# Kernel optimization log

Hardware: AMD Instinct MI355X
Metric: run time of the kernel (lower is better)

## Reference

```python
import jax, jax.numpy as jnp
import numpy as np

TEMPERATURE = 0.1
NUM_POS = 2


def _cross_entropy(logits, labels):
    # mean over batch of -log_softmax(logits)[i, labels[i]]
    logp = jax.nn.log_softmax(logits, axis=-1)
    return -jnp.take_along_axis(logp, labels[:, None], axis=1).mean()


def setup_inputs() -> dict:
    key = jax.random.key(0)
    k1, k2, k3 = jax.random.split(key, 3)
    B, D, Q = 4096, 256, 65536
    embedding = jax.random.normal(k1, (B, D), dtype=jnp.float32)
    preds = jax.random.normal(k2, (B, D), dtype=jnp.float32)
    queue = jax.random.normal(k3, (Q, D), dtype=jnp.float32)
    queue = queue / jnp.linalg.norm(queue, axis=1, keepdims=True)
    return {"embedding": embedding, "preds": preds, "queue": queue}


def reference(embedding, preds, queue):
    B = embedding.shape[0]
    half = B // NUM_POS
    labels = jnp.arange(half)  # single-trainer: dist_rank = 0

    # nearest-neighbor retrieval from the support queue (no-grad in original)
    sim = embedding @ queue.T                      # [B, Q]
    nearest = queue[jnp.argmax(sim, axis=1)]       # [B, D]

    nn_a, nn_b = nearest[:half], nearest[half:]
    preds_a, preds_b = preds[:half], preds[half:]

    logits_ab = (nn_a @ preds_b.T) / TEMPERATURE   # [half, half]
    logits_ba = (nn_b @ preds_a.T) / TEMPERATURE

    loss = _cross_entropy(logits_ab, labels) / 2 + _cross_entropy(logits_ba, labels) / 2
    return loss
```

## Files before the change

kernel.cpp:

```cpp
#include <hip/hip_runtime.h>
#include <hip/hip_bf16.h>
#include <stdint.h>

#define B_ROWS 4096
#define D_K    256
#define Q_ROWS 65536
#define HALF   2048

typedef __bf16 bf16x8 __attribute__((ext_vector_type(8)));
typedef float  f32x4  __attribute__((ext_vector_type(4)));
typedef int    v8i    __attribute__((ext_vector_type(8)));
typedef int    v4i    __attribute__((ext_vector_type(4)));
typedef unsigned short u16x8 __attribute__((ext_vector_type(8)));
typedef const __attribute__((address_space(1))) void* gptr1;
typedef __attribute__((address_space(3))) void* lptr3;

__device__ __forceinline__ unsigned int f32_ordered(float f) {
    unsigned int u = __float_as_uint(f);
    return (u & 0x80000000u) ? ~u : (u | 0x80000000u);
}

__device__ __forceinline__ unsigned short f2bf_rn(float f) {
    unsigned int u = __float_as_uint(f);
    u += 0x7FFFu + ((u >> 16) & 1u);
    return (unsigned short)(u >> 16);
}

#define EMB4  (B_ROWS * D_K / 4)
#define PRED4 (B_ROWS * D_K / 4)
#define QUE4  (Q_ROWS * D_K / 4)
#define PREP_THREADS ((EMB4 + PRED4 + QUE4) / 4)
__global__ __launch_bounds__(256) void prep_kernel(const float* __restrict__ emb,
                                                   const float* __restrict__ preds,
                                                   const float* __restrict__ queue,
                                                   unsigned char* __restrict__ emb8,
                                                   unsigned short* __restrict__ preds_bf,
                                                   unsigned char* __restrict__ queue8,
                                                   unsigned long long* __restrict__ amax,
                                                   float* __restrict__ out) {
    const int t  = blockIdx.x * 256 + threadIdx.x;
    const int g0 = t * 4;
    if (g0 < EMB4) {
        const float4* src = (const float4*)emb + g0;
        int4 o;
        { float4 v = src[0]; int u = __builtin_amdgcn_cvt_pk_fp8_f32(v.x, v.y, 0, false);
          o.x = __builtin_amdgcn_cvt_pk_fp8_f32(v.z, v.w, u, true); }
        { float4 v = src[1]; int u = __builtin_amdgcn_cvt_pk_fp8_f32(v.x, v.y, 0, false);
          o.y = __builtin_amdgcn_cvt_pk_fp8_f32(v.z, v.w, u, true); }
        { float4 v = src[2]; int u = __builtin_amdgcn_cvt_pk_fp8_f32(v.x, v.y, 0, false);
          o.z = __builtin_amdgcn_cvt_pk_fp8_f32(v.z, v.w, u, true); }
        { float4 v = src[3]; int u = __builtin_amdgcn_cvt_pk_fp8_f32(v.x, v.y, 0, false);
          o.w = __builtin_amdgcn_cvt_pk_fp8_f32(v.z, v.w, u, true); }
        ((int4*)emb8)[t] = o;
    } else if (g0 < EMB4 + PRED4) {
        const int off = g0 - EMB4;
        const float4* src = (const float4*)preds + off;
#pragma unroll
        for (int h = 0; h < 2; h++) {
            float4 v0 = src[2 * h], v1 = src[2 * h + 1];
            u16x8 o;
            o[0] = f2bf_rn(v0.x); o[1] = f2bf_rn(v0.y); o[2] = f2bf_rn(v0.z); o[3] = f2bf_rn(v0.w);
            o[4] = f2bf_rn(v1.x); o[5] = f2bf_rn(v1.y); o[6] = f2bf_rn(v1.z); o[7] = f2bf_rn(v1.w);
            ((u16x8*)preds_bf)[(off >> 1) + h] = o;
        }
    } else {
        const int off = g0 - EMB4 - PRED4;
        const float4* src = (const float4*)queue + off;
        int4 o;
        { float4 v = src[0]; int u = __builtin_amdgcn_cvt_pk_fp8_f32(v.x, v.y, 0, false);
          o.x = __builtin_amdgcn_cvt_pk_fp8_f32(v.z, v.w, u, true); }
        { float4 v = src[1]; int u = __builtin_amdgcn_cvt_pk_fp8_f32(v.x, v.y, 0, false);
          o.y = __builtin_amdgcn_cvt_pk_fp8_f32(v.z, v.w, u, true); }
        { float4 v = src[2]; int u = __builtin_amdgcn_cvt_pk_fp8_f32(v.x, v.y, 0, false);
          o.z = __builtin_amdgcn_cvt_pk_fp8_f32(v.z, v.w, u, true); }
        { float4 v = src[3]; int u = __builtin_amdgcn_cvt_pk_fp8_f32(v.x, v.y, 0, false);
          o.w = __builtin_amdgcn_cvt_pk_fp8_f32(v.z, v.w, u, true); }
        ((int4*)queue8)[off >> 2] = o;
    }
    if (t < B_ROWS) amax[t] = 0ull;
    if (t == 0) out[0] = 0.f;
}

#define BM 128
#define BN 128
#define NCHUNK 8
#define MFMA_FP8(av, bv, c) \
    __builtin_amdgcn_mfma_scale_f32_16x16x128_f8f6f4((av), (bv), (c), 0, 0, 0, 0x7F7F7F7F, 0, 0x7F7F7F7F)

#define WAITV(N) asm volatile("s_waitcnt vmcnt(" #N ")" ::: "memory")
#define BARRIER() do { __builtin_amdgcn_s_barrier(); \
                       asm volatile("" ::: "memory"); \
                       __builtin_amdgcn_sched_barrier(0); } while (0)

__global__ __launch_bounds__(256, 2) void sim_argmax_kernel(const unsigned char* __restrict__ A8,
                                                            const unsigned char* __restrict__ B8,
                                                            unsigned long long* __restrict__ amax) {
    __shared__ unsigned char sh[49152];

    const int tid  = threadIdx.x;
    const int wave = tid >> 6;
    const int lane = tid & 63;
    const int l15  = lane & 15;
    const int quad = lane >> 4;

    const int bid  = blockIdx.x;
    const int xcd  = bid & 7;
    const int j    = bid >> 3;
    const int blk_m = (j & 31) * BM;
    const int ngrp  = (j >> 5) * 8 + xcd;
    const int nbase = ngrp * (BN * NCHUNK);

    const int wave_m = (wave >> 1) * 64;
    const int wave_n = (wave & 1) * 64;

    {
        const unsigned char* gA = A8 + (size_t)(blk_m + (tid >> 4)) * D_K
                                     + (((tid & 15) ^ ((tid >> 4) & 15)) << 4);
#pragma unroll
        for (int jj = 0; jj < 8; jj++)
            __builtin_amdgcn_global_load_lds((gptr1)(gA + jj * 4096),
                                             (lptr3)&sh[jj * 4096 + wave * 1024], 16, 0, 0);
    }
    __syncthreads();

    const int pA = (quad * 2) ^ l15;
    v8i areg[2][4];
#pragma unroll
    for (int kt = 0; kt < 2; kt++) {
#pragma unroll
        for (int mi = 0; mi < 4; mi++) {
            const int _lo = (wave_m + mi * 16 + l15) * 256 + ((pA ^ (kt << 3)) << 4);
            v4i _x = *(const v4i*)&sh[_lo];
            v4i _y = *(const v4i*)&sh[_lo ^ 16];
            areg[kt][mi] = __builtin_shufflevector(_x, _y, 0, 1, 2, 3, 4, 5, 6, 7);
        }
    }
    __syncthreads();

    if ((bid >> 8) & 1) {
        __builtin_amdgcn_s_sleep(8);
        __builtin_amdgcn_s_sleep(4);
    }

    const unsigned char* gB = B8 + (size_t)(nbase + (tid >> 3)) * D_K
                                 + (((tid & 7) ^ ((tid >> 3) & 7)) << 4);

#define PREFB(T, BSOFF) do {                                                           \
        const int _off = ((T) >> 1) * (32 * D_K * 4) + ((T) & 1) * 128;                \
        _Pragma("unroll")                                                              \
        for (int _j = 0; _j < 4; _j++)                                                 \
            __builtin_amdgcn_global_load_lds((gptr1)(gB + _j * 8192 + _off),           \
                                             (lptr3)&sh[(BSOFF) + _j * 4096 + wave * 1024], 16, 0, 0); \
    } while (0)

    int Bbase[4];
#pragma unroll
    for (int ni = 0; ni < 4; ni++) Bbase[ni] = (wave_n + ni * 16 + l15) * 128;
    const int pB = (quad * 2) ^ (l15 & 7);

    int bestk[4][4];
#pragma unroll
    for (int mi = 0; mi < 4; mi++)
#pragma unroll
        for (int reg = 0; reg < 4; reg++) bestk[mi][reg] = 0x80000000;

    f32x4 acc[4][4];
    const f32x4 zero4 = (f32x4){0.f, 0.f, 0.f, 0.f};

#define COMPUTE0(BSOFF) do {                                                           \
        __builtin_amdgcn_s_setprio(1);                                                 \
        _Pragma("unroll")                                                              \
        for (int ni = 0; ni < 4; ni++) {                                               \
            const int _lo = (BSOFF) + Bbase[ni] + (pB << 4);                           \
            v4i _x = *(const v4i*)&sh[_lo];                                            \
            v4i _y = *(const v4i*)&sh[_lo ^ 16];                                       \
            v8i bv = __builtin_shufflevector(_x, _y, 0, 1, 2, 3, 4, 5, 6, 7);          \
            _Pragma("unroll")                                                          \
            for (int mi = 0; mi < 4; mi++)                                             \
                acc[mi][ni] = MFMA_FP8(areg[0][mi], bv, zero4);                        \
        }                                                                              \
        __builtin_amdgcn_s_setprio(0);                                                 \
    } while (0)

#define COMPUTE1(BSOFF) do {                                                           \
        __builtin_amdgcn_s_setprio(1);                                                 \
        _Pragma("unroll")                                                              \
        for (int ni = 0; ni < 4; ni++) {                                               \
            const int _lo = (BSOFF) + Bbase[ni] + (pB << 4);                           \
            v4i _x = *(const v4i*)&sh[_lo];                                            \
            v4i _y = *(const v4i*)&sh[_lo ^ 16];                                       \
            v8i bv = __builtin_shufflevector(_x, _y, 0, 1, 2, 3, 4, 5, 6, 7);          \
            _Pragma("unroll")                                                          \
            for (int mi = 0; mi < 4; mi++)                                             \
                acc[mi][ni] = MFMA_FP8(areg[1][mi], bv, acc[mi][ni]);                  \
        }                                                                              \
        __builtin_amdgcn_s_setprio(0);                                                 \
    } while (0)

#define FOLDK(PP) do {                                                                 \
        _Pragma("unroll")                                                              \
        for (int ni = 0; ni < 4; ni++) {                                               \
            const int _slot = 31 - ((PP) * 4 + ni);      \
            _Pragma("unroll")                                                          \
            for (int mi = 0; mi < 4; mi++)                                             \
                _Pragma("unroll")                                                      \
                for (int reg = 0; reg < 4; reg++) {                                    \
                    int ik = (__float_as_int(acc[mi][ni][reg]) & 0xFFFFFFE0) | _slot;  \
                    bestk[mi][reg] = max(bestk[mi][reg], ik);                          \
                }                                                                      \
        }                                                                              \
    } while (0)

#define ROT() do { int _t = b0; b0 = b1; b1 = b2; b2 = _t; } while (0)

    int b0 = 0, b1 = 16384, b2 = 32768;

    PREFB(0, b0);
    PREFB(1, b1);

#pragma unroll 1
    for (int p = 0; p < NCHUNK; ++p) {
        WAITV(4); BARRIER();
        if (p < NCHUNK - 1) PREFB(2 * p + 2, b2);
        if (p > 0) FOLDK(p - 1);
        COMPUTE0(b0);
        ROT();
        if (p < NCHUNK - 1) { WAITV(4); } else { WAITV(0); }
        BARRIER();
        if (p < NCHUNK - 1) PREFB(2 * p + 3, b2);
        COMPUTE1(b0);
        ROT();
    }
    FOLDK(NCHUNK - 1);

#pragma unroll
    for (int mi = 0; mi < 4; mi++) {
#pragma unroll
        for (int reg = 0; reg < 4; reg++) {
            unsigned u     = (unsigned)bestk[mi][reg];
            unsigned vbits = u & 0xFFFFFFE0u;
            int      pni   = 31 - (int)(u & 31u);
            int      col   = nbase + (pni >> 2) * BN + wave_n + ((pni & 3) << 4) + l15;
            unsigned ov    = (vbits & 0x80000000u) ? ~vbits : (vbits | 0x80000000u);
            unsigned long long key =
                ((unsigned long long)ov << 32) |
                (unsigned long long)(0xFFFFFFFFu - (unsigned)col);
#pragma unroll
            for (int m = 1; m < 16; m <<= 1) {
                unsigned long long o = __shfl_xor(key, m, 16);
                if (o > key) key = o;
            }
            if (l15 == mi * 4 + reg) {
                int row = blk_m + wave_m + mi * 16 + quad * 4 + reg;
                atomicMax(&amax[row], key);
            }
        }
    }
}

__global__ __launch_bounds__(512) void logits_ce_kernel(const unsigned long long* __restrict__ amax,
                                                        const float* __restrict__ queue_f32,
                                                        const unsigned short* __restrict__ preds_bf,
                                                        float* __restrict__ out) {
    const int gw   = blockIdx.x;
    const int tid  = threadIdx.x;
    const int wave = tid >> 6;
    const int lane = tid & 63;
    const int l15  = lane & 15;
    const int quad = lane >> 4;
    const int h    = gw >> 7;
    const int rowbase = gw * 16;
    const unsigned short* Bbase = preds_bf + (size_t)((1 - h) * HALF) * D_K;

    __shared__ float sm[8][16], sl[8][16], sd[8][16];

    unsigned idx = 0xFFFFFFFFu - (unsigned)(amax[rowbase + l15] & 0xFFFFFFFFull);
    const float* arow = queue_f32 + (size_t)idx * D_K;
    bf16x8 a[8];
#pragma unroll
    for (int kc = 0; kc < 8; kc++) {
        float4 f0 = *(const float4*)(arow + kc * 32 + quad * 8);
        float4 f1 = *(const float4*)(arow + kc * 32 + quad * 8 + 4);
        u16x8 t;
        t[0] = f2bf_rn(f0.x); t[1] = f2bf_rn(f0.y); t[2] = f2bf_rn(f0.z); t[3] = f2bf_rn(f0.w);
        t[4] = f2bf_rn(f1.x); t[5] = f2bf_rn(f1.y); t[6] = f2bf_rn(f1.z); t[7] = f2bf_rn(f1.w);
        a[kc] = *(const bf16x8*)&t;
    }

    float m_run[4], l_run[4], diag[4];
#pragma unroll
    for (int r = 0; r < 4; r++) { m_run[r] = -1e30f; l_run[r] = 0.f; diag[r] = -1e30f; }

    const int tdiag = gw & 127;
    for (int tt = 0; tt < 16; tt++) {
        const int t = wave * 16 + tt;
        f32x4 acc0 = (f32x4){0.f, 0.f, 0.f, 0.f};
        f32x4 acc1 = (f32x4){0.f, 0.f, 0.f, 0.f};
#pragma unroll
        for (int kc = 0; kc < 4; kc++) {
            bf16x8 b0 = *(const bf16x8*)&Bbase[(size_t)(t * 16 + l15) * D_K + kc * 32 + quad * 8];
            acc0 = __builtin_amdgcn_mfma_f32_16x16x32_bf16(a[kc], b0, acc0, 0, 0, 0);
            bf16x8 b1 = *(const bf16x8*)&Bbase[(size_t)(t * 16 + l15) * D_K + (kc + 4) * 32 + quad * 8];
            acc1 = __builtin_amdgcn_mfma_f32_16x16x32_bf16(a[kc + 4], b1, acc1, 0, 0, 0);
        }
        f32x4 acc = acc0 + acc1;
#pragma unroll
        for (int reg = 0; reg < 4; reg++) {
            float v = acc[reg] * 10.0f;
            if (t == tdiag && l15 == quad * 4 + reg) diag[reg] = v;
            float nm = fmaxf(m_run[reg], v);
            l_run[reg] = l_run[reg] * __expf(m_run[reg] - nm) + __expf(v - nm);
            m_run[reg] = nm;
        }
    }
#pragma unroll
    for (int reg = 0; reg < 4; reg++) {
#pragma unroll
        for (int m = 1; m < 16; m <<= 1) {
            float om = __shfl_xor(m_run[reg], m, 16);
            float ol = __shfl_xor(l_run[reg], m, 16);
            float od = __shfl_xor(diag[reg], m, 16);
            float nm = fmaxf(m_run[reg], om);
            l_run[reg] = l_run[reg] * __expf(m_run[reg] - nm) + ol * __expf(om - nm);
            m_run[reg] = nm;
            diag[reg] = fmaxf(diag[reg], od);
        }
        if (l15 == 0) {
            sm[wave][quad * 4 + reg] = m_run[reg];
            sl[wave][quad * 4 + reg] = l_run[reg];
            sd[wave][quad * 4 + reg] = diag[reg];
        }
    }
    __syncthreads();
    if (tid < 16) {
        float M = -1e30f, L = 0.f, Dg = -1e30f;
#pragma unroll
        for (int w = 0; w < 8; w++) {
            float mw = sm[w][tid], lw = sl[w][tid], dw = sd[w][tid];
            float nM = fmaxf(M, mw);
            L = L * __expf(M - nM) + lw * __expf(mw - nM);
            M = nM;
            Dg = fmaxf(Dg, dw);
        }
        float rl = (M + __logf(L)) - Dg;
#pragma unroll
        for (int m = 1; m < 16; m <<= 1) rl += __shfl_xor(rl, m, 16);
        if (tid == 0) atomicAdd(out, rl * (1.0f / (float)B_ROWS));
    }
}

extern "C" void kernel_launch(void* const* d_in, const int* in_sizes, int n_in,
                              void* d_out, int out_size, void* d_ws, size_t ws_size,
                              hipStream_t stream) {
    const float* emb   = (const float*)d_in[0];
    const float* preds = (const float*)d_in[1];
    const float* queue = (const float*)d_in[2];

    char* w = (char*)d_ws;
    unsigned long long* amax  = (unsigned long long*)w;
    unsigned char*  emb8      = (unsigned char*)(w + (1u << 20));
    unsigned short* preds_bf  = (unsigned short*)(w + (2u << 20));
    unsigned char*  queue8    = (unsigned char*)(w + (4u << 20));

    prep_kernel<<<dim3(PREP_THREADS / 256), 256, 0, stream>>>(
        emb, preds, queue, emb8, preds_bf, queue8, amax, (float*)d_out);
    sim_argmax_kernel<<<dim3((B_ROWS / BM) * (Q_ROWS / (BN * NCHUNK))), 256, 0, stream>>>(
        emb8, queue8, amax);
    logits_ce_kernel<<<dim3(B_ROWS / 16), 512, 0, stream>>>(
        amax, queue, preds_bf, (float*)d_out);
}
```

Before: 210.0 us.

## Load B fragments directly from global into registers, dropping LDS staging

Replaces the triple-buffered global_load_lds staging of queue tiles, along with its barriers and waitcnts, with direct per-lane global loads into register double buffers b0/b1 that feed the FP8 MFMAs. LDS shrinks to only what the A tile needs, and the staggered sleep for odd block groups is removed. This aims to cut LDS traffic and barrier synchronisation, and the smaller LDS footprint may allow more blocks per CU. In exchange, B data is no longer shared across the two wave rows, so each wave fetches its own copy from global/L2. The 32-byte per-lane loads are less coalesced, so load latency may be exposed behind less lookahead.

```diff
diff --git a/kernel.cpp b/kernel.cpp
--- a/kernel.cpp
+++ b/kernel.cpp
@@ -87,15 +87,10 @@
 #define MFMA_FP8(av, bv, c) \
     __builtin_amdgcn_mfma_scale_f32_16x16x128_f8f6f4((av), (bv), (c), 0, 0, 0, 0x7F7F7F7F, 0, 0x7F7F7F7F)
 
-#define WAITV(N) asm volatile("s_waitcnt vmcnt(" #N ")" ::: "memory")
-#define BARRIER() do { __builtin_amdgcn_s_barrier(); \
-                       asm volatile("" ::: "memory"); \
-                       __builtin_amdgcn_sched_barrier(0); } while (0)
-
 __global__ __launch_bounds__(256, 2) void sim_argmax_kernel(const unsigned char* __restrict__ A8,
                                                             const unsigned char* __restrict__ B8,
                                                             unsigned long long* __restrict__ amax) {
-    __shared__ unsigned char sh[49152];
+    __shared__ unsigned char sh[32768];
 
     const int tid  = threadIdx.x;
     const int wave = tid >> 6;
@@ -135,28 +130,11 @@
             areg[kt][mi] = __builtin_shufflevector(_x, _y, 0, 1, 2, 3, 4, 5, 6, 7);
         }
     }
-    __syncthreads();
-
-    if ((bid >> 8) & 1) {
-        __builtin_amdgcn_s_sleep(8);
-        __builtin_amdgcn_s_sleep(4);
-    }
-
-    const unsigned char* gB = B8 + (size_t)(nbase + (tid >> 3)) * D_K
-                                 + (((tid & 7) ^ ((tid >> 3) & 7)) << 4);
-
-#define PREFB(T, BSOFF) do {                                                           \
-        const int _off = ((T) >> 1) * (32 * D_K * 4) + ((T) & 1) * 128;                \
-        _Pragma("unroll")                                                              \
-        for (int _j = 0; _j < 4; _j++)                                                 \
-            __builtin_amdgcn_global_load_lds((gptr1)(gB + _j * 8192 + _off),           \
-                                             (lptr3)&sh[(BSOFF) + _j * 4096 + wave * 1024], 16, 0, 0); \
-    } while (0)
-
-    int Bbase[4];
-#pragma unroll
-    for (int ni = 0; ni < 4; ni++) Bbase[ni] = (wave_n + ni * 16 + l15) * 128;
-    const int pB = (quad * 2) ^ (l15 & 7);
+
+    const unsigned char* bptr0 = B8 + (size_t)(nbase + wave_n + l15) * 256 + quad * 32;
+    const unsigned char* bptr[4];
+#pragma unroll
+    for (int ni = 0; ni < 4; ni++) bptr[ni] = bptr0 + ni * 16 * 256;
 
     int bestk[4][4];
 #pragma unroll
@@ -167,14 +145,27 @@
     f32x4 acc[4][4];
     const f32x4 zero4 = (f32x4){0.f, 0.f, 0.f, 0.f};
 
-#define COMPUTE0(BSOFF) do {                                                           \
+    v4i b0[8], b1[8];
+
+#define LOADH(BUF, KT) do {                                                            \
+        _Pragma("unroll")                                                              \
+        for (int ni = 0; ni < 4; ni++) {                                               \
+            BUF[2 * ni]     = *(const v4i*)(bptr[ni] + (KT) * 128);                    \
+            BUF[2 * ni + 1] = *(const v4i*)(bptr[ni] + (KT) * 128 + 16);               \
+        }                                                                              \
+    } while (0)
+
+#define ADVB() do {                                                                    \
+        _Pragma("unroll")                                                              \
+        for (int ni = 0; ni < 4; ni++) bptr[ni] += BN * D_K;           \
+    } while (0)
+
+#define COMPUTE0(BUF) do {                                                             \
         __builtin_amdgcn_s_setprio(1);                                                 \
         _Pragma("unroll")                                                              \
         for (int ni = 0; ni < 4; ni++) {                                               \
-            const int _lo = (BSOFF) + Bbase[ni] + (pB << 4);                           \
-            v4i _x = *(const v4i*)&sh[_lo];                                            \
-            v4i _y = *(const v4i*)&sh[_lo ^ 16];                                       \
-            v8i bv = __builtin_shufflevector(_x, _y, 0, 1, 2, 3, 4, 5, 6, 7);          \
+            v8i bv = __builtin_shufflevector(BUF[2 * ni], BUF[2 * ni + 1],             \
+                                             0, 1, 2, 3, 4, 5, 6, 7);                  \
             _Pragma("unroll")                                                          \
             for (int mi = 0; mi < 4; mi++)                                             \
                 acc[mi][ni] = MFMA_FP8(areg[0][mi], bv, zero4);                        \
@@ -182,14 +173,12 @@
         __builtin_amdgcn_s_setprio(0);                                                 \
     } while (0)
 
-#define COMPUTE1(BSOFF) do {                                                           \
+#define COMPUTE1(BUF) do {                                                             \
         __builtin_amdgcn_s_setprio(1);                                                 \
         _Pragma("unroll")                                                              \
         for (int ni = 0; ni < 4; ni++) {                                               \
-            const int _lo = (BSOFF) + Bbase[ni] + (pB << 4);                           \
-            v4i _x = *(const v4i*)&sh[_lo];                                            \
-            v4i _y = *(const v4i*)&sh[_lo ^ 16];                                       \
-            v8i bv = __builtin_shufflevector(_x, _y, 0, 1, 2, 3, 4, 5, 6, 7);          \
+            v8i bv = __builtin_shufflevector(BUF[2 * ni], BUF[2 * ni + 1],             \
+                                             0, 1, 2, 3, 4, 5, 6, 7);                  \
             _Pragma("unroll")                                                          \
             for (int mi = 0; mi < 4; mi++)                                             \
                 acc[mi][ni] = MFMA_FP8(areg[1][mi], bv, acc[mi][ni]);                  \
@@ -211,25 +200,16 @@
         }                                                                              \
     } while (0)
 
-#define ROT() do { int _t = b0; b0 = b1; b1 = b2; b2 = _t; } while (0)
-
-    int b0 = 0, b1 = 16384, b2 = 32768;
-
-    PREFB(0, b0);
-    PREFB(1, b1);
+    LOADH(b0, 0);
 
 #pragma unroll 1
     for (int p = 0; p < NCHUNK; ++p) {
-        WAITV(4); BARRIER();
-        if (p < NCHUNK - 1) PREFB(2 * p + 2, b2);
+        LOADH(b1, 1);
         if (p > 0) FOLDK(p - 1);
         COMPUTE0(b0);
-        ROT();
-        if (p < NCHUNK - 1) { WAITV(4); } else { WAITV(0); }
-        BARRIER();
-        if (p < NCHUNK - 1) PREFB(2 * p + 3, b2);
-        COMPUTE1(b0);
-        ROT();
+        ADVB();
+        if (p < NCHUNK - 1) LOADH(b0, 0);
+        COMPUTE1(b1);
     }
     FOLDK(NCHUNK - 1);
 
```

After: 278.6 us. 1.33x slower.
